# Kernel tuning notes

Hardware: AMD Instinct MI355X
Metric: run time of the kernel (lower is better)

Reference implementation:

```python
import jax, jax.numpy as jnp
import numpy as np
import math

B, S, E = 4, 2048, 1024
H, D = 16, 64

def setup_inputs() -> dict:
    key = jax.random.key(0)
    ks = jax.random.split(key, 9)
    s = 0.02
    return {
        "x":  jax.random.normal(ks[0], (B, S, E), dtype=jnp.float32),
        "Wq": jax.random.normal(ks[1], (H, E, D), dtype=jnp.float32) * s,
        "Wk": jax.random.normal(ks[2], (H, E, D), dtype=jnp.float32) * s,
        "Wv": jax.random.normal(ks[3], (H, E, D), dtype=jnp.float32) * s,
        "bq": jax.random.normal(ks[4], (H, D), dtype=jnp.float32) * s,
        "bk": jax.random.normal(ks[5], (H, D), dtype=jnp.float32) * s,
        "bv": jax.random.normal(ks[6], (H, D), dtype=jnp.float32) * s,
        "Wo": jax.random.normal(ks[7], (H * D, E), dtype=jnp.float32) * s,
        "bo": jax.random.normal(ks[8], (E,), dtype=jnp.float32) * s,
    }

def reference(x, Wq, Wk, Wv, bq, bk, bv, Wo, bo):
    # batched per-head projections: [B,S,E] x [H,E,D] -> [B,H,S,D]
    Q = jnp.einsum('bse,hed->bhsd', x, Wq) + bq[None, :, None, :]
    K = jnp.einsum('bse,hed->bhsd', x, Wk) + bk[None, :, None, :]
    V = jnp.einsum('bse,hed->bhsd', x, Wv) + bv[None, :, None, :]
    scale = 1.0 / math.sqrt(D)
    scores = jnp.einsum('bhqd,bhkd->bhqk', Q, K) * scale  # [B,H,S,S]
    causal = jnp.tril(jnp.ones((S, S), dtype=bool))
    scores = jnp.where(causal, scores, -jnp.inf)
    attn = jax.nn.softmax(scores, axis=-1)
    ctx = jnp.einsum('bhqk,bhkd->bhqd', attn, V)  # [B,H,S,D]
    # concat heads along last dim == transpose to [B,S,H,D] then reshape
    conc = ctx.transpose(0, 2, 1, 3).reshape(B, S, H * D)
    out = conc @ Wo + bo  # dropout is identity in eval
    return out
```

## Files before the change

kernel.cpp:

```cpp
#include <hip/hip_runtime.h>
#include <stdint.h>

#define Bn 4
#define Sn 2048
#define En 1024
#define Hn 16
#define Dn 64

#define QSC 0.18033688011112f

typedef unsigned short u16;
typedef short s16x8 __attribute__((ext_vector_type(8)));
typedef float f32x4 __attribute__((ext_vector_type(4)));

#define MFMA16x16x32 __builtin_amdgcn_mfma_f32_16x16x32_bf16

__device__ __forceinline__ u16 f2bf(float f) {
  union { float f; uint32_t u; } v; v.f = f;
  uint32_t u = v.u;
  u += 0x7fffu + ((u >> 16) & 1u);
  return (u16)(u >> 16);
}
__device__ __forceinline__ uint32_t f2u(float f) {
  union { float f; uint32_t u; } v; v.f = f; return v.u;
}

#define AS1 __attribute__((address_space(1)))
#define AS3 __attribute__((address_space(3)))
__device__ __forceinline__ void gload_lds16(const void* g, void* l) {
  __builtin_amdgcn_global_load_lds((const AS1 uint32_t*)g, (AS3 uint32_t*)l, 16, 0, 0);
}

__global__ __launch_bounds__(256) void prep_all(
    const float4* __restrict__ x4, ushort4* __restrict__ xb4,
    const float* __restrict__ Wq, const float* __restrict__ Wk,
    const float* __restrict__ Wv, u16* __restrict__ WallT,
    const float* __restrict__ Wo, u16* __restrict__ WoT,
    const float* __restrict__ bq, const float* __restrict__ bk,
    const float* __restrict__ bv, float* __restrict__ biasA)
{
  __shared__ float t[64][65];
  const int tid = threadIdx.x;
  int blk = blockIdx.x;

  if (blk < 8192) {
    int i = blk * 256 + tid;
    float4 v = x4[i];
    ushort4 o;
    o.x = f2bf(v.x); o.y = f2bf(v.y); o.z = f2bf(v.z); o.w = f2bf(v.w);
    xb4[i] = o;
    return;
  }
  blk -= 8192;
  if (blk < 768) {
    const int e0 = (blk & 15) * 64;
    const int sh = blk >> 4;
    const int sec = sh >> 4, h = sh & 15;
    const float* W = (sec == 0) ? Wq : (sec == 1) ? Wk : Wv;
    const float* Wh = W + (size_t)h * En * Dn;
    const int d = tid & 63, er = tid >> 6;
#pragma unroll
    for (int ee = 0; ee < 64; ee += 4)
      t[ee + er][d] = Wh[(size_t)(e0 + ee + er) * Dn + d];
    __syncthreads();
    const int dd = tid >> 2, eo = (tid & 3) * 16;
    u16* dst = WallT + (size_t)(sec * 1024 + h * 64 + dd) * En + e0 + eo;
#pragma unroll
    for (int i = 0; i < 16; i += 4) {
      ushort4 o;
      o.x = f2bf(t[eo + i + 0][dd]);
      o.y = f2bf(t[eo + i + 1][dd]);
      o.z = f2bf(t[eo + i + 2][dd]);
      o.w = f2bf(t[eo + i + 3][dd]);
      *(ushort4*)(dst + i) = o;
    }
    return;
  }
  blk -= 768;
  if (blk < 256) {
    const int k0 = (blk & 15) * 64;
    const int n0 = (blk >> 4) * 64;
    const int c = tid & 63, r4 = tid >> 6;
#pragma unroll
    for (int rr = 0; rr < 64; rr += 4)
      t[rr + r4][c] = Wo[(size_t)(k0 + rr + r4) * En + n0 + c];
    __syncthreads();
    const int n = tid >> 2, ko = (tid & 3) * 16;
    u16* dst = WoT + (size_t)(n0 + n) * (Hn * Dn) + k0 + ko;
#pragma unroll
    for (int i = 0; i < 16; i += 4) {
      ushort4 o;
      o.x = f2bf(t[ko + i + 0][n]);
      o.y = f2bf(t[ko + i + 1][n]);
      o.z = f2bf(t[ko + i + 2][n]);
      o.w = f2bf(t[ko + i + 3][n]);
      *(ushort4*)(dst + i) = o;
    }
    return;
  }
  blk -= 256;
  int n = blk * 256 + tid;
  if (n < 3 * Hn * Dn) {
    int sec = n >> 10, rr = n & 1023;
    const float* bs = (sec == 0) ? bq : (sec == 1) ? bk : bv;
    biasA[n] = bs[rr];
  }
}

template<int MODE>
__global__ __launch_bounds__(256) void gemm_bt(
    const u16* __restrict__ A, const u16* __restrict__ Bt,
    const float* __restrict__ bias, int M, int N, int K,
    u16* __restrict__ q_out, u16* __restrict__ k_out, u16* __restrict__ v_out,
    float* __restrict__ f_out)
{
  extern __shared__ __align__(16) u16 smem[];

  const int tid  = threadIdx.x;
  const int L    = blockIdx.x;
  const int m0   = (L & 63) * 128;
  const int n0   = (L >> 6) * 128;
  const int w    = tid >> 6;
  const int lane = tid & 63;
  const int quad = lane >> 4;
  const int l15  = lane & 15;
  const int mbase = (w >> 1) * 64;
  const int nbase = (w & 1) * 64;
  const int swz   = (quad ^ ((l15 >> 1) & 3)) * 8;

  f32x4 acc[4][4];
#pragma unroll
  for (int i = 0; i < 4; ++i)
#pragma unroll
    for (int j = 0; j < 4; ++j)
      acc[i][j] = (f32x4){0.f, 0.f, 0.f, 0.f};

  auto stage = [&](int k0, int bf) {
    u16* lA = smem + bf * 4096;
    u16* lB = smem + 2 * 4096 + bf * 4096;
#pragma unroll
    for (int c = 0; c < 2; ++c) {
      int idx = c * 256 + tid;
      int row = idx >> 2, sl = idx & 3;
      int sg = sl ^ ((row >> 1) & 3);
      gload_lds16(A  + (size_t)(m0 + row) * K + k0 + sg * 8, &lA[idx * 8]);
      gload_lds16(Bt + (size_t)(n0 + row) * K + k0 + sg * 8, &lB[idx * 8]);
    }
  };

  stage(0, 0);
  int bf = 0;
  for (int k0 = 0; k0 < K; k0 += 32) {
    __syncthreads();
    if (k0 + 32 < K) stage(k0 + 32, bf ^ 1);
    const u16* lA = smem + bf * 4096;
    const u16* lB = smem + 2 * 4096 + bf * 4096;

    s16x8 af[4], bfr[4];
#pragma unroll
    for (int t = 0; t < 4; ++t) {
      af[t]  = *(const s16x8*)&lA[(mbase + t * 16 + l15) * 32 + swz];
      bfr[t] = *(const s16x8*)&lB[(nbase + t * 16 + l15) * 32 + swz];
    }
#pragma unroll
    for (int mt = 0; mt < 4; ++mt)
#pragma unroll
      for (int nt = 0; nt < 4; ++nt)
        acc[mt][nt] = MFMA16x16x32(af[mt], bfr[nt], acc[mt][nt], 0, 0, 0);
    bf ^= 1;
  }

  if (MODE == 0) {
    int sec = n0 >> 10;
    if (sec < 2) {
      float oscale = (sec == 0) ? QSC : 1.0f;
#pragma unroll
      for (int nt = 0; nt < 4; ++nt) {
        int col = n0 + nbase + nt * 16 + l15;
        float bv = bias[col];
        int rr = col & 1023;
        int h = rr >> 6, d = rr & 63;
        u16* dst = (sec == 0) ? q_out : k_out;
#pragma unroll
        for (int mt = 0; mt < 4; ++mt)
#pragma unroll
          for (int r = 0; r < 4; ++r) {
            int row = m0 + mbase + mt * 16 + quad * 4 + r;
            int b = row >> 11, s = row & 2047;
            dst[(((size_t)b * Hn + h) * Sn + s) * Dn + d] = f2bf((acc[mt][nt][r] + bv) * oscale);
          }
      }
    } else {
      __syncthreads();
      u16* lC = smem;
#pragma unroll
      for (int nt = 0; nt < 4; ++nt) {
        int cl = nbase + nt * 16 + l15;
        float bv = bias[n0 + cl];
#pragma unroll
        for (int mt = 0; mt < 4; ++mt)
#pragma unroll
          for (int r = 0; r < 4; ++r) {
            int rowl = mbase + mt * 16 + quad * 4 + r;
            lC[cl * 136 + rowl] = f2bf(acc[mt][nt][r] + bv);
          }
      }
      __syncthreads();
      int c  = tid >> 1, hh = tid & 1;
      int col = n0 + c;
      int h = (col >> 6) & 15, d = col & 63;
      int b = m0 >> 11;
      int s0 = (m0 & 2047) + hh * 64;
      const uint4* src = (const uint4*)&lC[c * 136 + hh * 64];
      uint4* dst = (uint4*)&v_out[(((size_t)b * Hn + h) * Dn + d) * Sn + s0];
#pragma unroll
      for (int i = 0; i < 8; ++i) dst[i] = src[i];
    }
  } else {
#pragma unroll
    for (int nt = 0; nt < 4; ++nt) {
      int col = n0 + nbase + nt * 16 + l15;
      float bv = bias[col];
#pragma unroll
      for (int mt = 0; mt < 4; ++mt)
#pragma unroll
        for (int r = 0; r < 4; ++r) {
          int row = m0 + mbase + mt * 16 + quad * 4 + r;
          f_out[(size_t)row * N + col] = acc[mt][nt][r] + bv;
        }
    }
  }
}

__global__ __launch_bounds__(256, 4) void flash_attn(
    const u16* __restrict__ Qb, const u16* __restrict__ Kb,
    const u16* __restrict__ Vt, u16* __restrict__ conc)
{
  __shared__ __align__(16) u16 lK[2][64 * 64];
  __shared__ __align__(16) u16 lV[2][64 * 64];
  __shared__ __align__(16) u16 lP[4][16 * 64];

  const int L   = blockIdx.x;
  const int bh  = L & 63;
  const int qt  = ((L >> 6) + (bh >> 2)) & 15;
  const int b   = bh >> 4, h = bh & 15;
  const int tid = threadIdx.x;
  const int w   = tid >> 6;
  const int lane = tid & 63;
  const int quad = lane >> 4;
  const int l15  = lane & 15;
  const int q0   = qt * 128;

  const u16* Qh = Qb + (size_t)bh * Sn * Dn;
  const u16* Kh = Kb + (size_t)bh * Sn * Dn;
  const u16* Vh = Vt + (size_t)bh * Dn * Sn;

  const int Q0m[2] = { q0 + w * 16, q0 + 64 + w * 16 };

  s16x8 aq[2][2];
#pragma unroll
  for (int m = 0; m < 2; ++m)
#pragma unroll
    for (int c = 0; c < 2; ++c)
      aq[m][c] = *(const s16x8*)&Qh[(size_t)(Q0m[m] + l15) * Dn + c * 32 + quad * 8];

  s16x8 kones;
#pragma unroll
  for (int i = 0; i < 8; ++i) kones[i] = (short)0x3F80;

  f32x4 acc[2][4];
#pragma unroll
  for (int m = 0; m < 2; ++m)
#pragma unroll
    for (int i = 0; i < 4; ++i) acc[m][i] = (f32x4){0.f, 0.f, 0.f, 0.f};
  const float NEG_INF = -__builtin_inff();
  float lrow[2] = {0.f, 0.f};

  const int sw0 = (quad ^ (l15 & 7)) * 8;
  const int sw1 = ((quad + 4) ^ (l15 & 7)) * 8;
  const int l7  = l15 & 7;

  const int ntiles = 2 * qt + 2;

  auto stage = [&](int kt) {
    int bufb = kt & 1;
    int kk0 = kt * 64;
#pragma unroll
    for (int c = 0; c < 2; ++c) {
      int idx = c * 256 + tid;
      int row = idx >> 3, sl = idx & 7;
      int sg = sl ^ (row & 7);
      gload_lds16(Kh + (size_t)(kk0 + row) * Dn + sg * 8, &lK[bufb][idx * 8]);
      gload_lds16(Vh + (size_t)row * Sn + kk0 + sg * 8, &lV[bufb][idx * 8]);
    }
  };

  stage(0);
  for (int kt = 0; kt < ntiles; ++kt) {
    const int kk0 = kt * 64;
    __syncthreads();
    if (kt + 1 < ntiles) stage(kt + 1);
    const u16* cK = lK[kt & 1];
    const u16* cV = lV[kt & 1];

#pragma unroll
    for (int m = 0; m < 2; ++m) {
      const int Q0 = Q0m[m];
      if (kk0 >= Q0 + 16) continue;

      f32x4 sc[4];
#pragma unroll
      for (int ct = 0; ct < 4; ++ct) {
        s16x8 bk0 = *(const s16x8*)&cK[(ct * 16 + l15) * 64 + sw0];
        s16x8 bk1 = *(const s16x8*)&cK[(ct * 16 + l15) * 64 + sw1];
        f32x4 z = (f32x4){0.f, 0.f, 0.f, 0.f};
        z = MFMA16x16x32(bk0, aq[m][0], z, 0, 0, 0);
        z = MFMA16x16x32(bk1, aq[m][1], z, 0, 0, 0);
        sc[ct] = z;
      }

      const int qg = Q0 + l15;
      if (kk0 + 63 > Q0) {
#pragma unroll
        for (int ct = 0; ct < 4; ++ct)
#pragma unroll
          for (int r = 0; r < 4; ++r) {
            int kkg = kk0 + ct * 16 + quad * 4 + r;
            sc[ct][r] = (kkg <= qg) ? sc[ct][r] : NEG_INF;
          }
      }

#pragma unroll
      for (int ct = 0; ct < 4; ++ct)
#pragma unroll
        for (int r = 0; r < 4; ++r)
          sc[ct][r] = __builtin_amdgcn_exp2f(sc[ct][r]);

      u16* Pw = &lP[w][0];
#pragma unroll
      for (int ct = 0; ct < 4; ++ct) {
        uint32_t d0 = __builtin_amdgcn_perm(f2u(sc[ct][1]), f2u(sc[ct][0]), 0x07060302);
        uint32_t d1 = __builtin_amdgcn_perm(f2u(sc[ct][3]), f2u(sc[ct][2]), 0x07060302);
        uint2 pk; pk.x = d0; pk.y = d1;
        int seg = (ct * 2 + (quad >> 1)) ^ l7;
        *(uint2*)&Pw[l15 * 64 + seg * 8 + (quad & 1) * 4] = pk;
      }
      __builtin_amdgcn_s_waitcnt(0xc07f);

      s16x8 ap0 = *(const s16x8*)&Pw[l15 * 64 + (quad ^ l7) * 8];
      s16x8 ap1 = *(const s16x8*)&Pw[l15 * 64 + ((quad + 4) ^ l7) * 8];

      f32x4 zl = (f32x4){0.f, 0.f, 0.f, 0.f};
      zl = MFMA16x16x32(kones, ap0, zl, 0, 0, 0);
      zl = MFMA16x16x32(kones, ap1, zl, 0, 0, 0);

#pragma unroll
      for (int dt = 0; dt < 4; ++dt) {
        s16x8 bv0 = *(const s16x8*)&cV[(dt * 16 + l15) * 64 + sw0];
        s16x8 bv1 = *(const s16x8*)&cV[(dt * 16 + l15) * 64 + sw1];
        acc[m][dt] = MFMA16x16x32(bv0, ap0, acc[m][dt], 0, 0, 0);
        acc[m][dt] = MFMA16x16x32(bv1, ap1, acc[m][dt], 0, 0, 0);
      }
      lrow[m] += zl[0];
    }
  }

#pragma unroll
  for (int m = 0; m < 2; ++m) {
    float inv = 1.0f / lrow[m];
    int qg = Q0m[m] + l15;
#pragma unroll
    for (int dt = 0; dt < 4; ++dt) {
      ushort4 o;
      o.x = f2bf(acc[m][dt][0] * inv);
      o.y = f2bf(acc[m][dt][1] * inv);
      o.z = f2bf(acc[m][dt][2] * inv);
      o.w = f2bf(acc[m][dt][3] * inv);
      *(ushort4*)&conc[((size_t)b * Sn + qg) * (Hn * Dn) + h * Dn + dt * 16 + quad * 4] = o;
    }
  }
}

extern "C" void kernel_launch(void* const* d_in, const int* in_sizes, int n_in,
                              void* d_out, int out_size, void* d_ws, size_t ws_size,
                              hipStream_t stream)
{
  const float* x  = (const float*)d_in[0];
  const float* Wq = (const float*)d_in[1];
  const float* Wk = (const float*)d_in[2];
  const float* Wv = (const float*)d_in[3];
  const float* bq = (const float*)d_in[4];
  const float* bk = (const float*)d_in[5];
  const float* bv = (const float*)d_in[6];
  const float* Wo = (const float*)d_in[7];
  const float* bo = (const float*)d_in[8];
  float* out = (float*)d_out;

  char* p = (char*)d_ws;
  u16* xb    = (u16*)p; p += (size_t)Bn * Sn * En * sizeof(u16);
  u16* WallT = (u16*)p; p += (size_t)3 * Hn * Dn * En * sizeof(u16);
  u16* WoT   = (u16*)p; p += (size_t)En * Hn * Dn * sizeof(u16);
  float* biasA = (float*)p; p += (size_t)3 * Hn * Dn * sizeof(float);
  u16* Qb    = (u16*)p; p += (size_t)Bn * Hn * Sn * Dn * sizeof(u16);
  u16* Kb    = (u16*)p; p += (size_t)Bn * Hn * Sn * Dn * sizeof(u16);
  u16* Vt    = (u16*)p; p += (size_t)Bn * Hn * Dn * Sn * sizeof(u16);
  u16* conc  = (u16*)p; p += (size_t)Bn * Sn * Hn * Dn * sizeof(u16);

  prep_all<<<9228, 256, 0, stream>>>((const float4*)x, (ushort4*)xb,
                                     Wq, Wk, Wv, WallT, Wo, WoT,
                                     bq, bk, bv, biasA);

  size_t smem0 = 128 * 136 * sizeof(u16);
  gemm_bt<0><<<24 * 64, 256, smem0, stream>>>(
      xb, WallT, biasA, Bn * Sn, 3 * Hn * Dn, En, Qb, Kb, Vt, nullptr);

  flash_attn<<<(Sn / 128) * Bn * Hn, 256, 0, stream>>>(Qb, Kb, Vt, conc);

  size_t smem1 = 4 * 4096 * sizeof(u16);
  gemm_bt<1><<<8 * 64, 256, smem1, stream>>>(
      conc, WoT, bo, Bn * Sn, En, Hn * Dn, nullptr, nullptr, nullptr, out);
}
```

Before: 251.2 us.

## Replace QKV projection GEMM with 256x256-tile, 512-thread phased MFMA kernel

```diff
diff --git a/kernel.cpp b/kernel.cpp
--- a/kernel.cpp
+++ b/kernel.cpp
@@ -171,51 +171,6 @@
   }
 
   if (MODE == 0) {
-    int sec = n0 >> 10;
-    if (sec < 2) {
-      float oscale = (sec == 0) ? QSC : 1.0f;
-#pragma unroll
-      for (int nt = 0; nt < 4; ++nt) {
-        int col = n0 + nbase + nt * 16 + l15;
-        float bv = bias[col];
-        int rr = col & 1023;
-        int h = rr >> 6, d = rr & 63;
-        u16* dst = (sec == 0) ? q_out : k_out;
-#pragma unroll
-        for (int mt = 0; mt < 4; ++mt)
-#pragma unroll
-          for (int r = 0; r < 4; ++r) {
-            int row = m0 + mbase + mt * 16 + quad * 4 + r;
-            int b = row >> 11, s = row & 2047;
-            dst[(((size_t)b * Hn + h) * Sn + s) * Dn + d] = f2bf((acc[mt][nt][r] + bv) * oscale);
-          }
-      }
-    } else {
-      __syncthreads();
-      u16* lC = smem;
-#pragma unroll
-      for (int nt = 0; nt < 4; ++nt) {
-        int cl = nbase + nt * 16 + l15;
-        float bv = bias[n0 + cl];
-#pragma unroll
-        for (int mt = 0; mt < 4; ++mt)
-#pragma unroll
-          for (int r = 0; r < 4; ++r) {
-            int rowl = mbase + mt * 16 + quad * 4 + r;
-            lC[cl * 136 + rowl] = f2bf(acc[mt][nt][r] + bv);
-          }
-      }
-      __syncthreads();
-      int c  = tid >> 1, hh = tid & 1;
-      int col = n0 + c;
-      int h = (col >> 6) & 15, d = col & 63;
-      int b = m0 >> 11;
-      int s0 = (m0 & 2047) + hh * 64;
-      const uint4* src = (const uint4*)&lC[c * 136 + hh * 64];
-      uint4* dst = (uint4*)&v_out[(((size_t)b * Hn + h) * Dn + d) * Sn + s0];
-#pragma unroll
-      for (int i = 0; i < 8; ++i) dst[i] = src[i];
-    }
   } else {
 #pragma unroll
     for (int nt = 0; nt < 4; ++nt) {
@@ -228,6 +183,188 @@
           int row = m0 + mbase + mt * 16 + quad * 4 + r;
           f_out[(size_t)row * N + col] = acc[mt][nt][r] + bv;
         }
+    }
+  }
+}
+
+#define LDA_Q(BASE, QM)                                                        \
+  do {                                                                         \
+    const u16* p_ = (BASE) + (wm * 128 + (QM) * 64 + l15) * 64;                \
+    _Pragma("unroll")                                                          \
+    for (int i_ = 0; i_ < 4; ++i_) {                                           \
+      af[i_][0] = *(const s16x8*)&p_[i_ * 1024 + sw0];                         \
+      af[i_][1] = *(const s16x8*)&p_[i_ * 1024 + sw1];                         \
+    }                                                                          \
+  } while (0)
+
+#define LDB_Q(BASE, QN, BF)                                                    \
+  do {                                                                         \
+    const u16* p_ = (BASE) + (wn * 64 + (QN) * 32 + l15) * 64;                 \
+    _Pragma("unroll")                                                          \
+    for (int j_ = 0; j_ < 2; ++j_) {                                           \
+      BF[j_][0] = *(const s16x8*)&p_[j_ * 1024 + sw0];                         \
+      BF[j_][1] = *(const s16x8*)&p_[j_ * 1024 + sw1];                         \
+    }                                                                          \
+  } while (0)
+
+#define PH_MM(QM, QN, BF)                                                      \
+  do {                                                                         \
+    __builtin_amdgcn_s_setprio(1);                                             \
+    _Pragma("unroll")                                                          \
+    for (int i_ = 0; i_ < 4; ++i_) {                                           \
+      _Pragma("unroll")                                                        \
+      for (int j_ = 0; j_ < 2; ++j_) {                                         \
+        acc[(QM) * 4 + i_][(QN) * 2 + j_] =                                    \
+            MFMA16x16x32(af[i_][0], BF[j_][0],                                 \
+                         acc[(QM) * 4 + i_][(QN) * 2 + j_], 0, 0, 0);          \
+        acc[(QM) * 4 + i_][(QN) * 2 + j_] =                                    \
+            MFMA16x16x32(af[i_][1], BF[j_][1],                                 \
+                         acc[(QM) * 4 + i_][(QN) * 2 + j_], 0, 0, 0);          \
+      }                                                                        \
+    }                                                                          \
+    __builtin_amdgcn_s_setprio(0);                                             \
+  } while (0)
+
+__global__ __launch_bounds__(512, 2) void gemm256_qkv(
+    const u16* __restrict__ A, const u16* __restrict__ Bt,
+    const float* __restrict__ bias,
+    u16* __restrict__ q_out, u16* __restrict__ k_out, u16* __restrict__ v_out)
+{
+  extern __shared__ __align__(16) u16 smem[];
+
+  const int tid  = threadIdx.x;
+  const int L    = blockIdx.x;
+  const int g    = (L & 7) * 48 + (L >> 3);
+  const int mi   = g / 12;
+  const int ni   = g - mi * 12;
+  const int m0   = mi * 256;
+  const int n0   = ni * 256;
+
+  const int w    = tid >> 6;
+  const int lane = tid & 63;
+  const int quad = lane >> 4;
+  const int l15  = lane & 15;
+  const int wm   = w >> 2;
+  const int wn   = w & 3;
+  const int l7   = l15 & 7;
+  const int sw0  = (quad ^ l7) * 8;
+  const int sw1  = ((quad + 4) ^ l7) * 8;
+
+  const int sr = tid >> 3, sl = tid & 7;
+  const int sg = sl ^ (sr & 7);
+  const u16* gA = A  + (size_t)(m0 + sr) * En + sg * 8;
+  const u16* gB = Bt + (size_t)(n0 + sr) * En + sg * 8;
+  const int lbase = tid * 8;
+
+  f32x4 acc[8][4];
+#pragma unroll
+  for (int i = 0; i < 8; ++i)
+#pragma unroll
+    for (int j = 0; j < 4; ++j)
+      acc[i][j] = (f32x4){0.f, 0.f, 0.f, 0.f};
+
+  s16x8 af[4][2], bf0[2][2], bf1[2][2];
+
+  auto stageA = [&](int k0, int db) {
+    u16* d = smem + db * 16384 + lbase;
+#pragma unroll
+    for (int c = 0; c < 4; ++c)
+      gload_lds16(gA + (size_t)c * 65536 + k0, d + c * 4096);
+  };
+  auto stageB = [&](int k0, int db) {
+    u16* d = smem + 32768 + db * 16384 + lbase;
+#pragma unroll
+    for (int c = 0; c < 4; ++c)
+      gload_lds16(gB + (size_t)c * 65536 + k0, d + c * 4096);
+  };
+
+  stageA(0, 0);
+  stageB(0, 0);
+  asm volatile("s_waitcnt vmcnt(0)" ::: "memory");
+  __builtin_amdgcn_s_barrier();
+
+  for (int t = 0; t < 16; ++t) {
+    const int db = t & 1;
+    const u16* cA = smem + db * 16384;
+    const u16* cB = smem + 32768 + db * 16384;
+    const int kn = (t + 1) * 64;
+
+    LDA_Q(cA, 0);
+    LDB_Q(cB, 0, bf0);
+    if (t < 15) stageA(kn, db ^ 1);
+    __builtin_amdgcn_s_barrier();
+    __builtin_amdgcn_s_waitcnt(0xc07f);
+    PH_MM(0, 0, bf0);
+    __builtin_amdgcn_s_barrier();
+
+    LDB_Q(cB, 1, bf1);
+    if (t < 15) stageB(kn, db ^ 1);
+    __builtin_amdgcn_s_barrier();
+    __builtin_amdgcn_s_waitcnt(0xc07f);
+    PH_MM(0, 1, bf1);
+    __builtin_amdgcn_s_barrier();
+
+    LDA_Q(cA, 1);
+    __builtin_amdgcn_s_barrier();
+    __builtin_amdgcn_s_waitcnt(0xc07f);
+    PH_MM(1, 1, bf1);
+    __builtin_amdgcn_s_barrier();
+
+    PH_MM(1, 0, bf0);
+    asm volatile("s_waitcnt vmcnt(0)" ::: "memory");
+    __builtin_amdgcn_s_barrier();
+  }
+
+  const int sec = n0 >> 10;
+  if (sec < 2) {
+    float osc = (sec == 0) ? QSC : 1.0f;
+    u16* dst = (sec == 0) ? q_out : k_out;
+#pragma unroll
+    for (int j = 0; j < 4; ++j) {
+      int col = n0 + wn * 64 + j * 16 + l15;
+      float bv = bias[col];
+      int rr = col & 1023;
+      int h = rr >> 6, d = rr & 63;
+#pragma unroll
+      for (int i = 0; i < 8; ++i)
+#pragma unroll
+        for (int r = 0; r < 4; ++r) {
+          int row = m0 + wm * 128 + i * 16 + quad * 4 + r;
+          int b = row >> 11, s = row & 2047;
+          dst[(((size_t)b * Hn + h) * Sn + s) * Dn + d] =
+              f2bf((acc[i][j][r] + bv) * osc);
+        }
+    }
+  } else {
+    __syncthreads();
+    u16* lC = smem;
+#pragma unroll
+    for (int j = 0; j < 4; ++j) {
+      int cl = wn * 64 + j * 16 + l15;
+      float bv = bias[n0 + cl];
+#pragma unroll
+      for (int i = 0; i < 8; ++i) {
+        int rowl = wm * 128 + i * 16 + quad * 4;
+        ushort4 o;
+        o.x = f2bf(acc[i][j][0] + bv);
+        o.y = f2bf(acc[i][j][1] + bv);
+        o.z = f2bf(acc[i][j][2] + bv);
+        o.w = f2bf(acc[i][j][3] + bv);
+        *(ushort4*)&lC[cl * 256 + (((rowl >> 3) ^ (cl & 31)) << 3) + (rowl & 7)] = o;
+      }
+    }
+    __syncthreads();
+    int c = tid >> 1, hh = tid & 1;
+    int col = n0 - 2048 + c;
+    int h = col >> 6, d = col & 63;
+    int b = m0 >> 11;
+    int s0 = (m0 & 2047) + hh * 128;
+    uint4* dst = (uint4*)&v_out[(((size_t)b * Hn + h) * Dn + d) * Sn + s0];
+#pragma unroll
+    for (int q = 0; q < 16; ++q) {
+      const uint4* src =
+          (const uint4*)&lC[c * 256 + (((hh * 16 + q) ^ (c & 31)) << 3)];
+      dst[q] = *src;
     }
   }
 }
@@ -410,9 +547,8 @@
                                      Wq, Wk, Wv, WallT, Wo, WoT,
                                      bq, bk, bv, biasA);
 
-  size_t smem0 = 128 * 136 * sizeof(u16);
-  gemm_bt<0><<<24 * 64, 256, smem0, stream>>>(
-      xb, WallT, biasA, Bn * Sn, 3 * Hn * Dn, En, Qb, Kb, Vt, nullptr);
+  size_t smemq = 4 * 16384 * sizeof(u16);
+  gemm256_qkv<<<32 * 12, 512, smemq, stream>>>(xb, WallT, biasA, Qb, Kb, Vt);
 
   flash_attn<<<(Sn / 128) * Bn * Hn, 256, 0, stream>>>(Qb, Kb, Vt, conc);
 
```

New measurement: 256.2 us. No clear change (+2.0%).

## Rewrite projection GEMMs with 32x32x16 MFMA, BK=64 tiles and XCD-aware block mapping

Applied to the files above, without the earlier changes.

```diff
diff --git a/kernel.cpp b/kernel.cpp
--- a/kernel.cpp
+++ b/kernel.cpp
@@ -12,8 +12,10 @@
 typedef unsigned short u16;
 typedef short s16x8 __attribute__((ext_vector_type(8)));
 typedef float f32x4 __attribute__((ext_vector_type(4)));
+typedef float f32x16 __attribute__((ext_vector_type(16)));
 
 #define MFMA16x16x32 __builtin_amdgcn_mfma_f32_16x16x32_bf16
+#define MFMA32x32x16 __builtin_amdgcn_mfma_f32_32x32x16_bf16
 
 __device__ __forceinline__ u16 f2bf(float f) {
   union { float f; uint32_t u; } v; v.f = f;
@@ -108,9 +110,9 @@
 }
 
 template<int MODE>
-__global__ __launch_bounds__(256) void gemm_bt(
+__global__ __launch_bounds__(256, 2) void gemm32(
     const u16* __restrict__ A, const u16* __restrict__ Bt,
-    const float* __restrict__ bias, int M, int N, int K,
+    const float* __restrict__ bias, int nTn,
     u16* __restrict__ q_out, u16* __restrict__ k_out, u16* __restrict__ v_out,
     float* __restrict__ f_out)
 {
@@ -118,116 +120,140 @@
 
   const int tid  = threadIdx.x;
   const int L    = blockIdx.x;
-  const int m0   = (L & 63) * 128;
-  const int n0   = (L >> 6) * 128;
+  const int tpx  = gridDim.x >> 3;
+  const int rl   = L >> 3;
+  const int mi   = (L & 7) * (tpx / nTn) + rl / nTn;
+  const int ni   = rl % nTn;
+  const int m0   = mi * 128;
+  const int n0   = ni * 128;
+
   const int w    = tid >> 6;
   const int lane = tid & 63;
-  const int quad = lane >> 4;
-  const int l15  = lane & 15;
-  const int mbase = (w >> 1) * 64;
-  const int nbase = (w & 1) * 64;
-  const int swz   = (quad ^ ((l15 >> 1) & 3)) * 8;
-
-  f32x4 acc[4][4];
-#pragma unroll
-  for (int i = 0; i < 4; ++i)
-#pragma unroll
-    for (int j = 0; j < 4; ++j)
-      acc[i][j] = (f32x4){0.f, 0.f, 0.f, 0.f};
-
-  auto stage = [&](int k0, int bf) {
-    u16* lA = smem + bf * 4096;
-    u16* lB = smem + 2 * 4096 + bf * 4096;
-#pragma unroll
-    for (int c = 0; c < 2; ++c) {
-      int idx = c * 256 + tid;
-      int row = idx >> 2, sl = idx & 3;
-      int sg = sl ^ ((row >> 1) & 3);
-      gload_lds16(A  + (size_t)(m0 + row) * K + k0 + sg * 8, &lA[idx * 8]);
-      gload_lds16(Bt + (size_t)(n0 + row) * K + k0 + sg * 8, &lB[idx * 8]);
+  const int wm   = w >> 1, wn = w & 1;
+  const int l31  = lane & 31;
+  const int half = lane >> 5;
+  const int l7   = lane & 7;
+
+  const int sr = tid >> 3, sl = tid & 7;
+  const int sg = sl ^ (sr & 7);
+  const u16* gA = A  + (size_t)(m0 + sr) * En + sg * 8;
+  const u16* gB = Bt + (size_t)(n0 + sr) * En + sg * 8;
+  const int lb = tid * 8;
+
+  f32x16 acc[2][2];
+#pragma unroll
+  for (int x = 0; x < 2; ++x)
+#pragma unroll
+    for (int y = 0; y < 2; ++y)
+#pragma unroll
+      for (int rg = 0; rg < 16; ++rg) acc[x][y][rg] = 0.f;
+
+  auto stage = [&](int t) {
+    const int db = t & 1;
+    const int k0 = t * 64;
+    u16* dA = smem + db * 8192 + lb;
+    u16* dB = smem + 16384 + db * 8192 + lb;
+#pragma unroll
+    for (int c = 0; c < 4; ++c) {
+      gload_lds16(gA + (size_t)(c * 32) * En + k0, dA + c * 2048);
+      gload_lds16(gB + (size_t)(c * 32) * En + k0, dB + c * 2048);
     }
   };
 
-  stage(0, 0);
-  int bf = 0;
-  for (int k0 = 0; k0 < K; k0 += 32) {
-    __syncthreads();
-    if (k0 + 32 < K) stage(k0 + 32, bf ^ 1);
-    const u16* lA = smem + bf * 4096;
-    const u16* lB = smem + 2 * 4096 + bf * 4096;
-
-    s16x8 af[4], bfr[4];
-#pragma unroll
-    for (int t = 0; t < 4; ++t) {
-      af[t]  = *(const s16x8*)&lA[(mbase + t * 16 + l15) * 32 + swz];
-      bfr[t] = *(const s16x8*)&lB[(nbase + t * 16 + l15) * 32 + swz];
-    }
-#pragma unroll
-    for (int mt = 0; mt < 4; ++mt)
-#pragma unroll
-      for (int nt = 0; nt < 4; ++nt)
-        acc[mt][nt] = MFMA16x16x32(af[mt], bfr[nt], acc[mt][nt], 0, 0, 0);
-    bf ^= 1;
+  stage(0);
+  asm volatile("s_waitcnt vmcnt(0)" ::: "memory");
+  __builtin_amdgcn_s_barrier();
+
+  for (int t = 0; t < 16; ++t) {
+    if (t < 15) stage(t + 1);
+    const u16* cA = smem + (t & 1) * 8192;
+    const u16* cB = smem + 16384 + (t & 1) * 8192;
+
+    s16x8 av[2][4], bv[2][4];
+#pragma unroll
+    for (int x = 0; x < 2; ++x) {
+      const u16* pa = cA + (size_t)(wm * 64 + x * 32 + l31) * 64;
+      const u16* pb = cB + (size_t)(wn * 64 + x * 32 + l31) * 64;
+#pragma unroll
+      for (int ks = 0; ks < 4; ++ks) {
+        av[x][ks] = *(const s16x8*)&pa[((2 * ks + half) ^ l7) * 8];
+        bv[x][ks] = *(const s16x8*)&pb[((2 * ks + half) ^ l7) * 8];
+      }
+    }
+#pragma unroll
+    for (int ks = 0; ks < 4; ++ks)
+#pragma unroll
+      for (int x = 0; x < 2; ++x)
+#pragma unroll
+        for (int y = 0; y < 2; ++y)
+          acc[x][y] = MFMA32x32x16(av[x][ks], bv[y][ks], acc[x][y], 0, 0, 0);
+
+    asm volatile("s_waitcnt vmcnt(0)" ::: "memory");
+    __builtin_amdgcn_s_barrier();
   }
 
   if (MODE == 0) {
-    int sec = n0 >> 10;
+    const int sec = n0 >> 10;
     if (sec < 2) {
-      float oscale = (sec == 0) ? QSC : 1.0f;
-#pragma unroll
-      for (int nt = 0; nt < 4; ++nt) {
-        int col = n0 + nbase + nt * 16 + l15;
-        float bv = bias[col];
-        int rr = col & 1023;
-        int h = rr >> 6, d = rr & 63;
-        u16* dst = (sec == 0) ? q_out : k_out;
-#pragma unroll
-        for (int mt = 0; mt < 4; ++mt)
-#pragma unroll
-          for (int r = 0; r < 4; ++r) {
-            int row = m0 + mbase + mt * 16 + quad * 4 + r;
-            int b = row >> 11, s = row & 2047;
-            dst[(((size_t)b * Hn + h) * Sn + s) * Dn + d] = f2bf((acc[mt][nt][r] + bv) * oscale);
+      const float osc = (sec == 0) ? QSC : 1.0f;
+      u16* dst = (sec == 0) ? q_out : k_out;
+      const int b = m0 >> 11;
+#pragma unroll
+      for (int y = 0; y < 2; ++y) {
+        int col = n0 + wn * 64 + y * 32 + l31;
+        float bvv = bias[col];
+        int rr = col & 1023, h = rr >> 6, d = rr & 63;
+#pragma unroll
+        for (int x = 0; x < 2; ++x) {
+          int rbase = (m0 & 2047) + wm * 64 + x * 32 + 4 * half;
+#pragma unroll
+          for (int rg = 0; rg < 16; ++rg) {
+            int s = rbase + (rg & 3) + 8 * (rg >> 2);
+            dst[(((size_t)b * Hn + h) * Sn + s) * Dn + d] =
+                f2bf((acc[x][y][rg] + bvv) * osc);
           }
+        }
       }
     } else {
+      u16* lC = smem;
+#pragma unroll
+      for (int y = 0; y < 2; ++y) {
+        int cl = wn * 64 + y * 32 + l31;
+        float bvv = bias[n0 + cl];
+#pragma unroll
+        for (int x = 0; x < 2; ++x) {
+          int rbase = wm * 64 + x * 32 + 4 * half;
+#pragma unroll
+          for (int rg = 0; rg < 16; ++rg)
+            lC[cl * 136 + rbase + (rg & 3) + 8 * (rg >> 2)] =
+                f2bf(acc[x][y][rg] + bvv);
+        }
+      }
       __syncthreads();
-      u16* lC = smem;
-#pragma unroll
-      for (int nt = 0; nt < 4; ++nt) {
-        int cl = nbase + nt * 16 + l15;
-        float bv = bias[n0 + cl];
-#pragma unroll
-        for (int mt = 0; mt < 4; ++mt)
-#pragma unroll
-          for (int r = 0; r < 4; ++r) {
-            int rowl = mbase + mt * 16 + quad * 4 + r;
-            lC[cl * 136 + rowl] = f2bf(acc[mt][nt][r] + bv);
-          }
-      }
-      __syncthreads();
-      int c  = tid >> 1, hh = tid & 1;
-      int col = n0 + c;
-      int h = (col >> 6) & 15, d = col & 63;
+      int c = tid >> 1, hh = tid & 1;
+      int colg = (n0 & 1023) + c;
+      int h = colg >> 6, d = colg & 63;
       int b = m0 >> 11;
       int s0 = (m0 & 2047) + hh * 64;
       const uint4* src = (const uint4*)&lC[c * 136 + hh * 64];
-      uint4* dst = (uint4*)&v_out[(((size_t)b * Hn + h) * Dn + d) * Sn + s0];
-#pragma unroll
-      for (int i = 0; i < 8; ++i) dst[i] = src[i];
+      uint4* dstv = (uint4*)&v_out[(((size_t)b * Hn + h) * Dn + d) * Sn + s0];
+#pragma unroll
+      for (int i = 0; i < 8; ++i) dstv[i] = src[i];
     }
   } else {
 #pragma unroll
-    for (int nt = 0; nt < 4; ++nt) {
-      int col = n0 + nbase + nt * 16 + l15;
-      float bv = bias[col];
-#pragma unroll
-      for (int mt = 0; mt < 4; ++mt)
-#pragma unroll
-        for (int r = 0; r < 4; ++r) {
-          int row = m0 + mbase + mt * 16 + quad * 4 + r;
-          f_out[(size_t)row * N + col] = acc[mt][nt][r] + bv;
+    for (int y = 0; y < 2; ++y) {
+      int col = n0 + wn * 64 + y * 32 + l31;
+      float bvv = bias[col];
+#pragma unroll
+      for (int x = 0; x < 2; ++x) {
+        int rbase = m0 + wm * 64 + x * 32 + 4 * half;
+#pragma unroll
+        for (int rg = 0; rg < 16; ++rg) {
+          int row = rbase + (rg & 3) + 8 * (rg >> 2);
+          f_out[(size_t)row * 1024 + col] = acc[x][y][rg] + bvv;
         }
+      }
     }
   }
 }
@@ -410,13 +436,13 @@
                                      Wq, Wk, Wv, WallT, Wo, WoT,
                                      bq, bk, bv, biasA);
 
-  size_t smem0 = 128 * 136 * sizeof(u16);
-  gemm_bt<0><<<24 * 64, 256, smem0, stream>>>(
-      xb, WallT, biasA, Bn * Sn, 3 * Hn * Dn, En, Qb, Kb, Vt, nullptr);
+  size_t smem32 = 4 * 8192 * sizeof(u16);
+
+  gemm32<0><<<1536, 256, smem32, stream>>>(xb, WallT, biasA, 24,
+                                           Qb, Kb, Vt, nullptr);
 
   flash_attn<<<(Sn / 128) * Bn * Hn, 256, 0, stream>>>(Qb, Kb, Vt, conc);
 
-  size_t smem1 = 4 * 4096 * sizeof(u16);
-  gemm_bt<1><<<8 * 64, 256, smem1, stream>>>(
-      conc, WoT, bo, Bn * Sn, En, Hn * Dn, nullptr, nullptr, nullptr, out);
-}
+  gemm32<1><<<512, 256, smem32, stream>>>(conc, WoT, bo, 8,
+                                          nullptr, nullptr, nullptr, out);
+}
```

Measured after the change: 264.7 us. 5.4% more time.

## Use dedicated 256x128-tile QKV projection GEMM with XCD-aware block mapping

Applied to the files above, without the earlier changes.

```diff
diff --git a/kernel.cpp b/kernel.cpp
--- a/kernel.cpp
+++ b/kernel.cpp
@@ -170,53 +170,7 @@
     bf ^= 1;
   }
 
-  if (MODE == 0) {
-    int sec = n0 >> 10;
-    if (sec < 2) {
-      float oscale = (sec == 0) ? QSC : 1.0f;
-#pragma unroll
-      for (int nt = 0; nt < 4; ++nt) {
-        int col = n0 + nbase + nt * 16 + l15;
-        float bv = bias[col];
-        int rr = col & 1023;
-        int h = rr >> 6, d = rr & 63;
-        u16* dst = (sec == 0) ? q_out : k_out;
-#pragma unroll
-        for (int mt = 0; mt < 4; ++mt)
-#pragma unroll
-          for (int r = 0; r < 4; ++r) {
-            int row = m0 + mbase + mt * 16 + quad * 4 + r;
-            int b = row >> 11, s = row & 2047;
-            dst[(((size_t)b * Hn + h) * Sn + s) * Dn + d] = f2bf((acc[mt][nt][r] + bv) * oscale);
-          }
-      }
-    } else {
-      __syncthreads();
-      u16* lC = smem;
-#pragma unroll
-      for (int nt = 0; nt < 4; ++nt) {
-        int cl = nbase + nt * 16 + l15;
-        float bv = bias[n0 + cl];
-#pragma unroll
-        for (int mt = 0; mt < 4; ++mt)
-#pragma unroll
-          for (int r = 0; r < 4; ++r) {
-            int rowl = mbase + mt * 16 + quad * 4 + r;
-            lC[cl * 136 + rowl] = f2bf(acc[mt][nt][r] + bv);
-          }
-      }
-      __syncthreads();
-      int c  = tid >> 1, hh = tid & 1;
-      int col = n0 + c;
-      int h = (col >> 6) & 15, d = col & 63;
-      int b = m0 >> 11;
-      int s0 = (m0 & 2047) + hh * 64;
-      const uint4* src = (const uint4*)&lC[c * 136 + hh * 64];
-      uint4* dst = (uint4*)&v_out[(((size_t)b * Hn + h) * Dn + d) * Sn + s0];
-#pragma unroll
-      for (int i = 0; i < 8; ++i) dst[i] = src[i];
-    }
-  } else {
+  {
 #pragma unroll
     for (int nt = 0; nt < 4; ++nt) {
       int col = n0 + nbase + nt * 16 + l15;
@@ -228,6 +182,130 @@
           int row = m0 + mbase + mt * 16 + quad * 4 + r;
           f_out[(size_t)row * N + col] = acc[mt][nt][r] + bv;
         }
+    }
+  }
+}
+
+__global__ __launch_bounds__(256, 3) void gemm_qkv2(
+    const u16* __restrict__ A, const u16* __restrict__ Bt,
+    const float* __restrict__ bias,
+    u16* __restrict__ q_out, u16* __restrict__ k_out, u16* __restrict__ v_out)
+{
+  extern __shared__ __align__(16) u16 smem[];
+
+  const int tid  = threadIdx.x;
+  const int L    = blockIdx.x;
+  const int xcd  = L & 7;
+  const int rl   = L >> 3;
+  const int mi   = rl / 3;
+  const int ni   = xcd * 3 + (rl - mi * 3);
+  const int m0   = mi * 256;
+  const int n0   = ni * 128;
+
+  const int w    = tid >> 6;
+  const int lane = tid & 63;
+  const int quad = lane >> 4;
+  const int l15  = lane & 15;
+  const int wm   = w >> 1;
+  const int wn   = w & 1;
+  const int swz  = (quad ^ ((l15 >> 1) & 3)) * 8;
+
+  f32x4 acc[8][4];
+#pragma unroll
+  for (int i = 0; i < 8; ++i)
+#pragma unroll
+    for (int j = 0; j < 4; ++j)
+      acc[i][j] = (f32x4){0.f, 0.f, 0.f, 0.f};
+
+  auto stage = [&](int t) {
+    const int db = t & 1;
+    const int k0 = t * 32;
+    u16* lA = smem + db * 8192;
+    u16* lB = smem + 16384 + db * 4096;
+#pragma unroll
+    for (int c = 0; c < 4; ++c) {
+      int idx = c * 256 + tid;
+      int row = idx >> 2, sl = idx & 3;
+      int sg = sl ^ ((row >> 1) & 3);
+      gload_lds16(A + (size_t)(m0 + row) * En + k0 + sg * 8, &lA[idx * 8]);
+    }
+#pragma unroll
+    for (int c = 0; c < 2; ++c) {
+      int idx = c * 256 + tid;
+      int row = idx >> 2, sl = idx & 3;
+      int sg = sl ^ ((row >> 1) & 3);
+      gload_lds16(Bt + (size_t)(n0 + row) * En + k0 + sg * 8, &lB[idx * 8]);
+    }
+  };
+
+  stage(0);
+  for (int t = 0; t < 32; ++t) {
+    __syncthreads();
+    if (t + 1 < 32) stage(t + 1);
+    const u16* cA = smem + (t & 1) * 8192;
+    const u16* cB = smem + 16384 + (t & 1) * 4096;
+
+    s16x8 bf4[4];
+#pragma unroll
+    for (int nt = 0; nt < 4; ++nt)
+      bf4[nt] = *(const s16x8*)&cB[(wn * 64 + nt * 16 + l15) * 32 + swz];
+#pragma unroll
+    for (int mt = 0; mt < 8; ++mt) {
+      s16x8 af = *(const s16x8*)&cA[(wm * 128 + mt * 16 + l15) * 32 + swz];
+#pragma unroll
+      for (int nt = 0; nt < 4; ++nt)
+        acc[mt][nt] = MFMA16x16x32(af, bf4[nt], acc[mt][nt], 0, 0, 0);
+    }
+  }
+
+  const int sec = n0 >> 10;
+  if (sec < 2) {
+    const float osc = (sec == 0) ? QSC : 1.0f;
+    u16* dst = (sec == 0) ? q_out : k_out;
+#pragma unroll
+    for (int nt = 0; nt < 4; ++nt) {
+      int col = n0 + wn * 64 + nt * 16 + l15;
+      float bv = bias[col];
+      int rr = col & 1023;
+      int h = rr >> 6, d = rr & 63;
+#pragma unroll
+      for (int mt = 0; mt < 8; ++mt)
+#pragma unroll
+        for (int r = 0; r < 4; ++r) {
+          int row = m0 + wm * 128 + mt * 16 + quad * 4 + r;
+          int b = row >> 11, s = row & 2047;
+          dst[(((size_t)b * Hn + h) * Sn + s) * Dn + d] =
+              f2bf((acc[mt][nt][r] + bv) * osc);
+        }
+    }
+  } else {
+    __syncthreads();
+    u16* lC = smem;
+    const int b = m0 >> 11;
+#pragma unroll
+    for (int p = 0; p < 2; ++p) {
+      if (wm == p) {
+#pragma unroll
+        for (int nt = 0; nt < 4; ++nt) {
+          int cl = wn * 64 + nt * 16 + l15;
+          float bv = bias[n0 + cl];
+#pragma unroll
+          for (int mt = 0; mt < 8; ++mt)
+#pragma unroll
+            for (int r = 0; r < 4; ++r)
+              lC[cl * 136 + mt * 16 + quad * 4 + r] = f2bf(acc[mt][nt][r] + bv);
+        }
+      }
+      __syncthreads();
+      int c = tid >> 1, hh = tid & 1;
+      int colg = (n0 & 1023) + c;
+      int h = colg >> 6, d = colg & 63;
+      int s0 = (m0 & 2047) + p * 128 + hh * 64;
+      const uint4* src = (const uint4*)&lC[c * 136 + hh * 64];
+      uint4* dstv = (uint4*)&v_out[(((size_t)b * Hn + h) * Dn + d) * Sn + s0];
+#pragma unroll
+      for (int i = 0; i < 8; ++i) dstv[i] = src[i];
+      if (p == 0) __syncthreads();
     }
   }
 }
@@ -410,9 +488,8 @@
                                      Wq, Wk, Wv, WallT, Wo, WoT,
                                      bq, bk, bv, biasA);
 
-  size_t smem0 = 128 * 136 * sizeof(u16);
-  gemm_bt<0><<<24 * 64, 256, smem0, stream>>>(
-      xb, WallT, biasA, Bn * Sn, 3 * Hn * Dn, En, Qb, Kb, Vt, nullptr);
+  size_t smemq = 24576 * sizeof(u16);
+  gemm_qkv2<<<768, 256, smemq, stream>>>(xb, WallT, biasA, Qb, Kb, Vt);
 
   flash_attn<<<(Sn / 128) * Bn * Hn, 256, 0, stream>>>(Qb, Kb, Vt, conc);
 
```

Result: no change. 254.9 us (+1.5%).
